# Optimization experiments

Measured on AMD Instinct MI355X. Metric: run time of the kernel, lower is better.

## Reference

```python
import jax, jax.numpy as jnp
import numpy as np

THRESH = 0.3

def _quantize_ternary(s):
    # straight-through ternary: forward value is q, gradient is identity
    q = jnp.where(s > THRESH, 1.0, jnp.where(s < -THRESH, -1.0, 0.0))
    return s + jax.lax.stop_gradient(q - s)

def setup_inputs() -> dict:
    key = jax.random.key(0)
    k1, k2, k3 = jax.random.split(key, 3)
    B, D, T, C = 32768, 1024, 16, 1000
    x = jax.random.normal(k1, (B, D), dtype=jnp.float32)
    sigs_raw = jax.random.normal(k2, (T, D), dtype=jnp.float32) * 0.5
    # per-tile Linear(d_model, n_classes): weight [C, D], bias [C]
    W = jax.random.normal(k3, (T, C, D), dtype=jnp.float32) / np.sqrt(D)
    b = jnp.zeros((T, C), dtype=jnp.float32)
    return {"x": x, "sigs_raw": sigs_raw, "W": W, "b": b}

def reference(x, sigs_raw, W, b):
    sigs = _quantize_ternary(sigs_raw)          # [T, D] ternary values
    scores = x @ sigs.T                          # [B, T]
    tile_indices = jnp.argmax(scores, axis=-1)   # [B] top-1 routing
    n_tiles = W.shape[0]
    logits = jnp.zeros((x.shape[0], W.shape[1]), dtype=x.dtype)  # [B, C]
    # static loop over tiles: masked per-expert linear, combined by select
    for t in range(n_tiles):
        m = (tile_indices == t)[:, None]         # [B, 1]
        yt = x @ W[t].T + b[t]                   # [B, C]
        logits = jnp.where(m, yt, logits)
    return logits, tile_indices
```

## Files before the change

### kernel.cpp

```cpp
#include <hip/hip_runtime.h>

#define NBROWS 32768
#define ND 1024
#define NT 16
#define NC 1000
#define NHB 128
#define MAX_RB128 272

typedef short short8 __attribute__((ext_vector_type(8)));
typedef float f32x4 __attribute__((ext_vector_type(4)));
typedef unsigned short ushort_t;

typedef __attribute__((address_space(1))) const unsigned int* gas_t;
typedef __attribute__((address_space(3))) unsigned int* las_t;

__device__ __forceinline__ void async_copy16(const void* g, void* l) {
  __builtin_amdgcn_global_load_lds((gas_t)g, (las_t)l, 16, 0, 0);
}

__device__ __forceinline__ unsigned f2bf(float f) {
  unsigned u = __float_as_uint(f);
  u += 0x7FFFu + ((u >> 16) & 1u);
  return u >> 16;
}
__device__ __forceinline__ unsigned pk2(float a, float b) {
  return f2bf(a) | (f2bf(b) << 16);
}
__device__ __forceinline__ int swz(int row) { return (row & 3) ^ ((row >> 2) & 3); }

__global__ __launch_bounds__(512) void fused_pre(
    const float* __restrict__ x, const float* __restrict__ sigs_raw,
    int* __restrict__ tidx, float* __restrict__ out_idx,
    const float* __restrict__ W, ushort_t* __restrict__ wbf,
    ushort_t* __restrict__ xbf) {
  __shared__ signed char s_lds[NT * ND];
  int tid = threadIdx.x;
  int bid = blockIdx.x;
  if (bid >= 4096) {
    if (!wbf) return;
    size_t e = (((size_t)(bid - 4096)) * 512 + tid) * 8;
    int t = (int)(e >> 20);
    int rem = (int)(e & 1048575);
    int col = rem >> 10, k = rem & 1023;
    uint4 o;
    if (col < NC) {
      const float* src = W + ((size_t)t * NC + col) * ND + k;
      float4 a = *(const float4*)src;
      float4 b = *(const float4*)(src + 4);
      o = make_uint4(pk2(a.x, a.y), pk2(a.z, a.w), pk2(b.x, b.y), pk2(b.z, b.w));
    } else {
      o = make_uint4(0, 0, 0, 0);
    }
    *(uint4*)(wbf + e) = o;
    return;
  }
  for (int i = tid; i < NT * ND; i += 512) {
    float s = sigs_raw[i];
    s_lds[i] = (s > 0.3f) ? 1 : ((s < -0.3f) ? -1 : 0);
  }
  __syncthreads();
  int lane = tid & 63;
  int row = bid * 8 + (tid >> 6);
  const float* xr = x + (size_t)row * ND + lane * 16;
  float4 v0 = *(const float4*)(xr);
  float4 v1 = *(const float4*)(xr + 4);
  float4 v2 = *(const float4*)(xr + 8);
  float4 v3 = *(const float4*)(xr + 12);
  float xv[16] = {v0.x, v0.y, v0.z, v0.w, v1.x, v1.y, v1.z, v1.w,
                  v2.x, v2.y, v2.z, v2.w, v3.x, v3.y, v3.z, v3.w};
  if (xbf) {
    ushort_t* xo = xbf + (size_t)row * ND + lane * 16;
    *(uint4*)(xo) = make_uint4(pk2(v0.x, v0.y), pk2(v0.z, v0.w), pk2(v1.x, v1.y), pk2(v1.z, v1.w));
    *(uint4*)(xo + 8) = make_uint4(pk2(v2.x, v2.y), pk2(v2.z, v2.w), pk2(v3.x, v3.y), pk2(v3.z, v3.w));
  }
  float best = 0.0f;
  int bt = 0;
#pragma unroll
  for (int t = 0; t < NT; t++) {
    int4 sc = *(const int4*)(s_lds + t * ND + lane * 16);
    int wa[4] = {sc.x, sc.y, sc.z, sc.w};
    float p = 0.0f;
#pragma unroll
    for (int wi = 0; wi < 4; wi++)
#pragma unroll
      for (int bi = 0; bi < 4; bi++)
        p = fmaf((float)(signed char)(wa[wi] >> (8 * bi)), xv[wi * 4 + bi], p);
#pragma unroll
    for (int o = 32; o > 0; o >>= 1) p += __shfl_xor(p, o);
    if (t == 0 || p > best) { best = p; bt = t; }
  }
  if (lane == 0) {
    tidx[row] = bt;
    out_idx[row] = (float)bt;
  }
}

__global__ __launch_bounds__(256) void trix_hist(const int* __restrict__ tidx,
                                                 int* __restrict__ blkhist) {
  __shared__ int h[NT];
  int tid = threadIdx.x;
  if (tid < NT) h[tid] = 0;
  __syncthreads();
  int t = tidx[blockIdx.x * 256 + tid];
  atomicAdd(&h[t], 1);
  __syncthreads();
  if (tid < NT) blkhist[blockIdx.x * NT + tid] = h[tid];
}

__global__ __launch_bounds__(256) void trix_prefix(const int* __restrict__ blkhist,
                                                   int* __restrict__ blkbase,
                                                   int* __restrict__ meta) {
  __shared__ int part[NT][16];
  int tid = threadIdx.x;
  int t = tid >> 4, g = tid & 15;
  int s = 0;
  for (int b = g; b < NHB; b += 16) s += blkhist[b * NT + t];
  part[t][g] = s;
  __syncthreads();
  if (tid == 0) {
    int off = 0, cb2 = 0;
    for (int tt = 0; tt < NT; tt++) {
      int c = 0;
#pragma unroll
      for (int gg = 0; gg < 16; gg++) c += part[tt][gg];
      meta[tt] = c;
      meta[16 + tt] = off;
      meta[50 + tt] = cb2;
      off += c;
      cb2 += (c + 127) >> 7;
    }
    meta[32] = off;
    meta[66] = cb2;
  }
  __syncthreads();
  if (tid < NT) {
    int run = meta[16 + tid];
    for (int b = 0; b < NHB; b++) {
      blkbase[b * NT + tid] = run;
      run += blkhist[b * NT + tid];
    }
  }
}

__global__ __launch_bounds__(256) void trix_scatter(const int* __restrict__ tidx,
                                                    const int* __restrict__ blkbase,
                                                    int* __restrict__ rowlist) {
  __shared__ int h[NT];
  int tid = threadIdx.x;
  if (tid < NT) h[tid] = 0;
  __syncthreads();
  int row = blockIdx.x * 256 + tid;
  int t = tidx[row];
  int r = atomicAdd(&h[t], 1);
  rowlist[blkbase[blockIdx.x * NT + t] + r] = row;
}

__global__ __launch_bounds__(256, 3) void trix_gemm7(
    const ushort_t* __restrict__ xbf, const ushort_t* __restrict__ wbf,
    const float* __restrict__ bias, const int* __restrict__ meta,
    const int* __restrict__ rowlist, float* __restrict__ out) {
  __shared__ __align__(16) ushort_t A_lds[128 * 64];
  __shared__ __align__(16) ushort_t B_lds[128 * 64];
  __shared__ int rl[128];
  int bid = blockIdx.x;
  int w = (bid & 7) * 272 + (bid >> 3);
  int nb = w & 7, rb = w >> 3;
  if (rb >= meta[66]) return;
  int t = 0;
  while (t < NT - 1 && rb >= meta[51 + t]) t++;
  int row0 = meta[16 + t] + (rb - meta[50 + t]) * 128;
  int cnt = meta[17 + t] - row0;
  if (cnt > 128) cnt = 128;
  int tid = threadIdx.x;
  if (tid < 128) rl[tid] = rowlist[(tid < cnt) ? (row0 + tid) : row0];
  __syncthreads();

  int lane = tid & 63, wv = tid >> 6;
  int srow = lane >> 3;
  int schunk = ((lane & 7) ^ srow) * 8;
  const ushort_t* aS[4];
  const ushort_t* bS[4];
#pragma unroll
  for (int j = 0; j < 4; j++) {
    aS[j] = xbf + (size_t)rl[wv * 32 + j * 8 + srow] * ND + schunk;
    bS[j] = wbf + ((size_t)t << 20) + (size_t)(nb * 128 + wv * 32 + j * 8 + srow) * ND + schunk;
  }
  int ldst = wv * 2048 + lane * 8;

  int wr = wv >> 1, wc = wv & 1;
  int rsel = lane & 15, ksl = lane >> 4, rx = rsel & 7;
  int sl0 = (ksl ^ rx) * 8;
  int sl1 = ((4 + ksl) ^ rx) * 8;
  int aoff = (wr * 64 + rsel) * 64;
  int boff = (wc * 64 + rsel) * 64;

  f32x4 acc[4][4] = {};

#define STAGE(KTL)                                            \
  _Pragma("unroll") for (int j = 0; j < 4; j++) {             \
    async_copy16(aS[j] + (KTL) * 64, &A_lds[ldst + j * 512]); \
    async_copy16(bS[j] + (KTL) * 64, &B_lds[ldst + j * 512]); \
  }

  STAGE(0);
  asm volatile("s_waitcnt vmcnt(0)" ::: "memory");
  __builtin_amdgcn_s_barrier();

#pragma unroll 1
  for (int kt = 0; kt < 16; ++kt) {
    short8 af[4][2], bf2[4][2];
#pragma unroll
    for (int m = 0; m < 4; m++) {
      af[m][0] = *(const short8*)(&A_lds[aoff + m * 1024 + sl0]);
      af[m][1] = *(const short8*)(&A_lds[aoff + m * 1024 + sl1]);
    }
#pragma unroll
    for (int n = 0; n < 4; n++) {
      bf2[n][0] = *(const short8*)(&B_lds[boff + n * 1024 + sl0]);
      bf2[n][1] = *(const short8*)(&B_lds[boff + n * 1024 + sl1]);
    }
    asm volatile("s_waitcnt lgkmcnt(0)" ::: "memory");
    __builtin_amdgcn_sched_barrier(0);
    __builtin_amdgcn_s_barrier();
    if (kt < 15) STAGE(kt + 1);
    __builtin_amdgcn_s_setprio(1);
#pragma unroll
    for (int n = 0; n < 4; n++)
#pragma unroll
      for (int m = 0; m < 4; m++) {
        acc[m][n] = __builtin_amdgcn_mfma_f32_16x16x32_bf16(af[m][0], bf2[n][0], acc[m][n], 0, 0, 0);
        acc[m][n] = __builtin_amdgcn_mfma_f32_16x16x32_bf16(af[m][1], bf2[n][1], acc[m][n], 0, 0, 0);
      }
    __builtin_amdgcn_s_setprio(0);
    asm volatile("s_waitcnt vmcnt(0)" ::: "memory");
    __builtin_amdgcn_s_barrier();
  }
#undef STAGE

  float bv[4];
  int bcol[4];
#pragma unroll
  for (int n = 0; n < 4; ++n) {
    bcol[n] = nb * 128 + wc * 64 + n * 16 + rsel;
    bv[n] = (bcol[n] < NC) ? bias[t * NC + bcol[n]] : 0.0f;
  }
#pragma unroll
  for (int m = 0; m < 4; ++m) {
#pragma unroll
    for (int r = 0; r < 4; ++r) {
      int lr = wr * 64 + m * 16 + ksl * 4 + r;
      if (lr < cnt) {
        size_t ob = (size_t)rl[lr] * NC;
#pragma unroll
        for (int n = 0; n < 4; ++n)
          if (bcol[n] < NC) out[ob + bcol[n]] = acc[m][n][r] + bv[n];
      }
    }
  }
}

__global__ __launch_bounds__(256) void trix_gemm_fb(
    const float* __restrict__ x, const float* __restrict__ W,
    const float* __restrict__ bias, const int* __restrict__ meta,
    const int* __restrict__ rowlist, float* __restrict__ out) {
  __shared__ __align__(16) unsigned char aT[128 * 64];
  __shared__ __align__(16) unsigned char bT[128 * 64];
  __shared__ int rl[128];
  int nb = blockIdx.x, rb = blockIdx.y;
  if (rb >= meta[66]) return;
  int t = 0;
  while (t < NT - 1 && rb >= meta[51 + t]) t++;
  int row0 = meta[16 + t] + (rb - meta[50 + t]) * 128;
  int cnt = meta[17 + t] - row0;
  if (cnt > 128) cnt = 128;
  int tid = threadIdx.x;
  if (tid < 128) rl[tid] = rowlist[(tid < cnt) ? (row0 + tid) : row0];
  __syncthreads();
  int half = tid & 1, rloc = tid >> 1;
  const float* xp = x + (size_t)rl[rloc] * ND + half * 16;
  int wn = nb * 128 + rloc;
  if (wn > NC - 1) wn = NC - 1;
  const float* wp = W + ((size_t)t * NC + wn) * ND + half * 16;
  int sw = swz(rloc);
  unsigned char* aw0 = aT + rloc * 64 + (((half * 2 + 0) ^ sw) << 4);
  unsigned char* aw1 = aT + rloc * 64 + (((half * 2 + 1) ^ sw) << 4);
  unsigned char* bw0 = bT + rloc * 64 + (((half * 2 + 0) ^ sw) << 4);
  unsigned char* bw1 = bT + rloc * 64 + (((half * 2 + 1) ^ sw) << 4);
  int lane = tid & 63, wv = tid >> 6;
  int wr = wv >> 1, wc = wv & 1;
  int rsel = lane & 15, slot = lane >> 4;
  f32x4 acc[4][4] = {};
  for (int k0 = 0; k0 < ND; k0 += 32) {
    const float* xk = xp + k0;
    const float* wk = wp + k0;
    float4 a0 = *(const float4*)(xk);
    float4 a1 = *(const float4*)(xk + 4);
    float4 a2 = *(const float4*)(xk + 8);
    float4 a3 = *(const float4*)(xk + 12);
    float4 b0 = *(const float4*)(wk);
    float4 b1 = *(const float4*)(wk + 4);
    float4 b2 = *(const float4*)(wk + 8);
    float4 b3 = *(const float4*)(wk + 12);
    *(uint4*)aw0 = make_uint4(pk2(a0.x, a0.y), pk2(a0.z, a0.w), pk2(a1.x, a1.y), pk2(a1.z, a1.w));
    *(uint4*)aw1 = make_uint4(pk2(a2.x, a2.y), pk2(a2.z, a2.w), pk2(a3.x, a3.y), pk2(a3.z, a3.w));
    *(uint4*)bw0 = make_uint4(pk2(b0.x, b0.y), pk2(b0.z, b0.w), pk2(b1.x, b1.y), pk2(b1.z, b1.w));
    *(uint4*)bw1 = make_uint4(pk2(b2.x, b2.y), pk2(b2.z, b2.w), pk2(b3.x, b3.y), pk2(b3.z, b3.w));
    __syncthreads();
    short8 af2[4], bfr[4];
#pragma unroll
    for (int i = 0; i < 4; i++) {
      int arr = wr * 64 + i * 16 + rsel;
      af2[i] = *(const short8*)(aT + arr * 64 + ((slot ^ swz(arr)) << 4));
      int brr = wc * 64 + i * 16 + rsel;
      bfr[i] = *(const short8*)(bT + brr * 64 + ((slot ^ swz(brr)) << 4));
    }
#pragma unroll
    for (int mi = 0; mi < 4; mi++)
#pragma unroll
      for (int ni = 0; ni < 4; ni++)
        acc[mi][ni] = __builtin_amdgcn_mfma_f32_16x16x32_bf16(af2[mi], bfr[ni], acc[mi][ni], 0, 0, 0);
    __syncthreads();
  }
#pragma unroll
  for (int mi = 0; mi < 4; mi++) {
#pragma unroll
    for (int r = 0; r < 4; r++) {
      int rloc2 = wr * 64 + mi * 16 + slot * 4 + r;
      if (rloc2 < cnt) {
        size_t obase = (size_t)rl[rloc2] * NC;
#pragma unroll
        for (int ni = 0; ni < 4; ni++) {
          int col = nb * 128 + wc * 64 + ni * 16 + rsel;
          if (col < NC) out[obase + col] = acc[mi][ni][r] + bias[t * NC + col];
        }
      }
    }
  }
}

extern "C" void kernel_launch(void* const* d_in, const int* in_sizes, int n_in,
                              void* d_out, int out_size, void* d_ws, size_t ws_size,
                              hipStream_t stream) {
  const float* x = (const float*)d_in[0];
  const float* sigs = (const float*)d_in[1];
  const float* W = (const float*)d_in[2];
  const float* bias = (const float*)d_in[3];
  float* out = (float*)d_out;

  const size_t XBF_B = (size_t)NBROWS * ND * 2;
  const size_t WBF_B = (size_t)NT * 1024 * ND * 2;
  bool fast = ws_size >= XBF_B + WBF_B + (1 << 20);

  char* wsb = (char*)d_ws;
  ushort_t* xbf = nullptr;
  ushort_t* wbf = nullptr;
  int* tidx;
  if (fast) {
    xbf = (ushort_t*)wsb;
    wbf = (ushort_t*)(wsb + XBF_B);
    tidx = (int*)(wsb + XBF_B + WBF_B);
  } else {
    tidx = (int*)wsb;
  }
  int* rowlist = tidx + NBROWS;
  int* meta = rowlist + NBROWS;
  int* blkhist = meta + 80;
  int* blkbase = blkhist + NHB * NT;

  fused_pre<<<8192, 512, 0, stream>>>(x, sigs, tidx, out + (size_t)NBROWS * NC, W, wbf, xbf);
  trix_hist<<<NHB, 256, 0, stream>>>(tidx, blkhist);
  trix_prefix<<<1, 256, 0, stream>>>(blkhist, blkbase, meta);
  trix_scatter<<<NHB, 256, 0, stream>>>(tidx, blkbase, rowlist);
  if (fast) {
    trix_gemm7<<<8 * MAX_RB128, 256, 0, stream>>>(xbf, wbf, bias, meta, rowlist, out);
  } else {
    trix_gemm_fb<<<dim3(8, MAX_RB128), 256, 0, stream>>>(x, W, bias, meta, rowlist, out);
  }
}
```

Measured before the change: 176.3 us.

## Double-buffer LDS tiles in grouped GEMM with two-stage async prefetch

Changes the routed expert GEMM from a single-buffered LDS tile to a double-buffered ping-pong scheme. Two K-tiles are prefetched ahead, and the wait is relaxed to vmcnt(8) so one stage's global loads stay in flight during compute. Dummy loads keep the vmcnt accounting uniform in the last iterations. LDS use doubles, so launch bounds drop from 3 to 2 blocks per CU, trading occupancy for deeper overlap of load latency with MFMA work.

New measurement: 193.2 us. 9.6% more time.

```diff
diff --git a/kernel.cpp b/kernel.cpp
--- a/kernel.cpp
+++ b/kernel.cpp
@@ -155,12 +155,13 @@
   rowlist[blkbase[blockIdx.x * NT + t] + r] = row;
 }
 
-__global__ __launch_bounds__(256, 3) void trix_gemm7(
+__global__ __launch_bounds__(256, 2) void trix_gemm8(
     const ushort_t* __restrict__ xbf, const ushort_t* __restrict__ wbf,
     const float* __restrict__ bias, const int* __restrict__ meta,
     const int* __restrict__ rowlist, float* __restrict__ out) {
-  __shared__ __align__(16) ushort_t A_lds[128 * 64];
-  __shared__ __align__(16) ushort_t B_lds[128 * 64];
+  __shared__ __align__(16) ushort_t A_lds[2 * 8192];
+  __shared__ __align__(16) ushort_t B_lds[2 * 8192];
+  __shared__ __align__(16) ushort_t dmy[512];
   __shared__ int rl[128];
   int bid = blockIdx.x;
   int w = (bid & 7) * 272 + (bid >> 3);
@@ -196,33 +197,45 @@
 
   f32x4 acc[4][4] = {};
 
-#define STAGE(KTL)                                            \
-  _Pragma("unroll") for (int j = 0; j < 4; j++) {             \
-    async_copy16(aS[j] + (KTL) * 64, &A_lds[ldst + j * 512]); \
-    async_copy16(bS[j] + (KTL) * 64, &B_lds[ldst + j * 512]); \
-  }
-
-  STAGE(0);
-  asm volatile("s_waitcnt vmcnt(0)" ::: "memory");
+#define STAGE(KTL, P)                                                      \
+  _Pragma("unroll") for (int j = 0; j < 4; j++) {                          \
+    async_copy16(aS[j] + (KTL) * 64, &A_lds[(P) * 8192 + ldst + j * 512]); \
+    async_copy16(bS[j] + (KTL) * 64, &B_lds[(P) * 8192 + ldst + j * 512]); \
+  }
+#define STAGE_DMY                                       \
+  _Pragma("unroll") for (int j = 0; j < 8; j++) {       \
+    async_copy16(xbf + lane * 8, &dmy[0]);              \
+  }
+
+  STAGE(0, 0);
+  STAGE(1, 1);
+  asm volatile("s_waitcnt vmcnt(8)" ::: "memory");
   __builtin_amdgcn_s_barrier();
 
 #pragma unroll 1
   for (int kt = 0; kt < 16; ++kt) {
+    int p = kt & 1;
+    const ushort_t* Ab = &A_lds[p * 8192];
+    const ushort_t* Bb = &B_lds[p * 8192];
     short8 af[4][2], bf2[4][2];
 #pragma unroll
     for (int m = 0; m < 4; m++) {
-      af[m][0] = *(const short8*)(&A_lds[aoff + m * 1024 + sl0]);
-      af[m][1] = *(const short8*)(&A_lds[aoff + m * 1024 + sl1]);
+      af[m][0] = *(const short8*)(Ab + aoff + m * 1024 + sl0);
+      af[m][1] = *(const short8*)(Ab + aoff + m * 1024 + sl1);
     }
 #pragma unroll
     for (int n = 0; n < 4; n++) {
-      bf2[n][0] = *(const short8*)(&B_lds[boff + n * 1024 + sl0]);
-      bf2[n][1] = *(const short8*)(&B_lds[boff + n * 1024 + sl1]);
+      bf2[n][0] = *(const short8*)(Bb + boff + n * 1024 + sl0);
+      bf2[n][1] = *(const short8*)(Bb + boff + n * 1024 + sl1);
     }
     asm volatile("s_waitcnt lgkmcnt(0)" ::: "memory");
     __builtin_amdgcn_sched_barrier(0);
     __builtin_amdgcn_s_barrier();
-    if (kt < 15) STAGE(kt + 1);
+    if (kt < 14) {
+      STAGE(kt + 2, p);
+    } else {
+      STAGE_DMY;
+    }
     __builtin_amdgcn_s_setprio(1);
 #pragma unroll
     for (int n = 0; n < 4; n++)
@@ -232,10 +245,12 @@
         acc[m][n] = __builtin_amdgcn_mfma_f32_16x16x32_bf16(af[m][1], bf2[n][1], acc[m][n], 0, 0, 0);
       }
     __builtin_amdgcn_s_setprio(0);
-    asm volatile("s_waitcnt vmcnt(0)" ::: "memory");
+    asm volatile("s_waitcnt vmcnt(8)" ::: "memory");
+    __builtin_amdgcn_sched_barrier(0);
     __builtin_amdgcn_s_barrier();
   }
 #undef STAGE
+#undef STAGE_DMY
 
   float bv[4];
   int bcol[4];
@@ -372,7 +387,7 @@
   trix_prefix<<<1, 256, 0, stream>>>(blkhist, blkbase, meta);
   trix_scatter<<<NHB, 256, 0, stream>>>(tidx, blkbase, rowlist);
   if (fast) {
-    trix_gemm7<<<8 * MAX_RB128, 256, 0, stream>>>(xbf, wbf, bias, meta, rowlist, out);
+    trix_gemm8<<<8 * MAX_RB128, 256, 0, stream>>>(xbf, wbf, bias, meta, rowlist, out);
   } else {
     trix_gemm_fb<<<dim3(8, MAX_RB128), 256, 0, stream>>>(x, W, bias, meta, rowlist, out);
   }
```
